# Kernel tuning notes

Measured on AMD Instinct MI355X. Metric: run time of the kernel, lower is better.

## Reference

```python
import jax, jax.numpy as jnp
import numpy as np

# conv hyperparams matching init_kwargs (kernel=3, stride=1, pad=1, dilation=1, dg=1)
KH = KW = 3
SH = SW = 1
PH = PW = 1
DH = DW = 1


def setup_inputs() -> dict:
    key = jax.random.key(0)
    k1, k2, k3 = jax.random.split(key, 3)
    N, C, H, W = 4, 64, 128, 128
    OC, KN = 64, KH * KW
    x = jax.random.normal(k1, (N, C, H, W), jnp.float32)
    # offset channels: deformable_groups * kernel_n * 2, ordered (y, x) per point
    offset = jax.random.normal(k2, (N, KN * 2, H, W), jnp.float32)
    weight = jax.random.normal(k3, (OC, C, KN), jnp.float32) * 0.05
    return {"x": x, "offset": offset, "weight": weight}


def _bilinear(img, ix, iy):
    # img: (C, H, W); ix, iy: (KN, OH, OW) pixel coords; align_corners=True, zeros padding
    H, W = img.shape[1], img.shape[2]
    x0 = jnp.floor(ix)
    y0 = jnp.floor(iy)
    x1 = x0 + 1.0
    y1 = y0 + 1.0
    wx1 = ix - x0
    wx0 = 1.0 - wx1
    wy1 = iy - y0
    wy0 = 1.0 - wy1

    def gather(xc, yc, w):
        xi = jnp.clip(xc, 0, W - 1).astype(jnp.int32)
        yi = jnp.clip(yc, 0, H - 1).astype(jnp.int32)
        m = ((xc >= 0) & (xc <= W - 1) & (yc >= 0) & (yc <= H - 1)).astype(img.dtype)
        return img[:, yi, xi] * (w * m)[None]  # (C, KN, OH, OW)

    return (gather(x0, y0, wx0 * wy0) + gather(x1, y0, wx1 * wy0)
            + gather(x0, y1, wx0 * wy1) + gather(x1, y1, wx1 * wy1))


def reference(x, offset, weight):
    N, C, H, W = x.shape
    KN = weight.shape[2]
    OH, OW = offset.shape[2], offset.shape[3]
    half_h = (H - 1) / 2.0
    half_w = (W - 1) / 2.0
    # base mesh in normalized [-1,1] coords (same for every kernel point, per source)
    ys = jnp.arange(OH, dtype=x.dtype) * SH - PH + ((KH - 1) // 2) * DH
    xs = jnp.arange(OW, dtype=x.dtype) * SW - PW + ((KW - 1) // 2) * DW
    base_gy = (ys - half_h) / half_h  # (OH,)
    base_gx = (xs - half_w) / half_w  # (OW,)
    off = offset.reshape(N, KN, 2, OH, OW)
    gy = base_gy[None, None, :, None] + off[:, :, 0] / half_h  # (N, KN, OH, OW)
    gx = base_gx[None, None, None, :] + off[:, :, 1] / half_w
    # back to pixel coords (align_corners=True)
    ix = (gx + 1.0) * half_w
    iy = (gy + 1.0) * half_h
    sampled = jax.vmap(_bilinear)(x, ix, iy)  # (N, C, KN, OH, OW)
    # weight (OC, C, KN) contracted over (C, KN); note: source forward never adds bias
    out = jnp.einsum('oik,nikhw->nohw', weight, sampled)
    return out
```

## Files before the change

kernel.cpp:

```cpp
#include <hip/hip_runtime.h>
#include <hip/hip_bf16.h>


#define NB 4
#define CI 64
#define HH 128
#define WW 128
#define OCH 64
#define KNN 9
#define HW (HH * WW)

typedef unsigned int u32;
typedef unsigned short u16;
typedef __attribute__((ext_vector_type(8))) short bf16x8;
typedef __attribute__((ext_vector_type(4))) float f32x4;

typedef const __attribute__((address_space(1))) u32* gas_ptr;
typedef __attribute__((address_space(3))) u32* las_ptr;

__device__ inline u16 f2bf(float f) {
    u32 u = __float_as_uint(f);
    return (u16)((u + 0x7fffu + ((u >> 16) & 1u)) >> 16);
}
__device__ inline u32 pk2(float lo, float hi) {
    return (u32)f2bf(lo) | ((u32)f2bf(hi) << 16);
}
__device__ inline void up2(u32 u, float& lo, float& hi) {
    lo = __uint_as_float(u << 16);
    hi = __uint_as_float(u & 0xffff0000u);
}
__device__ inline void gload_lds16(const u16* g, u16* s) {
    __builtin_amdgcn_global_load_lds((gas_ptr)g, (las_ptr)s, 16, 0, 0);
}

__global__ __launch_bounds__(256) void prep_kernel(const float* __restrict__ x,
                                                   const float* __restrict__ w,
                                                   u16* __restrict__ xT,
                                                   u16* __restrict__ wf) {
    __shared__ float T[64 * 68];
    const int tid = threadIdx.x;
    if (blockIdx.x < NB * 256) {
        const int n = blockIdx.x >> 8;
        const int hw0 = (blockIdx.x & 255) << 6;
#pragma unroll
        for (int jj = 0; jj < 4; jj++) {
            int c = (tid >> 4) + (jj << 4);
            int hwq = (tid & 15) << 2;
            float4 v = *(const float4*)&x[(((n << 6) + c) << 14) + hw0 + hwq];
            *(float4*)&T[c * 68 + hwq] = v;
        }
        __syncthreads();
        const int hw_l = tid >> 2;
        const int cb = (tid & 3) << 4;
        u32 ou[8];
#pragma unroll
        for (int k = 0; k < 8; k++) {
            ou[k] = pk2(T[(cb + 2 * k) * 68 + hw_l], T[(cb + 2 * k + 1) * 68 + hw_l]);
        }
        u16* dst = xT + ((size_t)((n << 14) + hw0 + hw_l) << 6) + cb;
        *(uint4*)dst = make_uint4(ou[0], ou[1], ou[2], ou[3]);
        *(uint4*)(dst + 8) = make_uint4(ou[4], ou[5], ou[6], ou[7]);
    } else {
        int i = (blockIdx.x - NB * 256) * 256 + tid;
        if (i < KNN * 2 * 4 * 64 * 8) {
            int j = i & 7, l = (i >> 3) & 63, strip = (i >> 9) & 3,
                chunk = (i >> 11) & 1, kn = i >> 12;
            int oc = strip * 16 + (l & 15);
            int c = chunk * 32 + ((l >> 4) & 3) * 8 + j;
            wf[i] = f2bf(w[(oc * CI + c) * KNN + kn]);
        }
    }
}

__global__ __launch_bounds__(256, 2) void dcn_main_kernel(const u16* __restrict__ xT,
                                                          const float* __restrict__ off,
                                                          const u16* __restrict__ wf,
                                                          float* __restrict__ out) {
    __shared__ __align__(16) u16 Abuf[KNN * 4096];
    const int tid = threadIdx.x;
    const int l = tid & 63;
    const int wv = tid >> 6;

    {
        const u16* g = wf + tid * 8;
        u16* s = Abuf + tid * 8;
#pragma unroll
        for (int i = 0; i < 18; i++) {
            gload_lds16(g + i * 2048, s + i * 2048);
        }
    }

    const int n = blockIdx.x >> 8;
    const int patch = blockIdx.x & 255;
    const int py = ((patch >> 4) << 3), px = ((patch & 15) << 3);
    const int qy = ((wv >> 1) << 2), qx = ((wv & 1) << 2);
    const int col = l & 15;
    const int oh = py + qy + (col >> 2);
    const int ow = px + qx + (col & 3);
    const int rr = (oh << 7) + ow;
    const int cbase = (l >> 4) << 3;
    const u16* xTn = xT + ((size_t)n << 20);
    const float* offn = off + n * (2 * KNN * HW);

    float offy[KNN], offx[KNN];
#pragma unroll
    for (int kn = 0; kn < KNN; kn++) {
        offy[kn] = offn[(2 * kn) * HW + rr];
        offx[kn] = offn[(2 * kn + 1) * HW + rr];
    }

    __syncthreads();

    f32x4 acc[4] = {{0, 0, 0, 0}, {0, 0, 0, 0}, {0, 0, 0, 0}, {0, 0, 0, 0}};

#pragma unroll
    for (int kn = 0; kn < KNN; kn++) {
        float iy = (float)oh + offy[kn], ix = (float)ow + offx[kn];
        float y0f = floorf(iy), x0f = floorf(ix);
        float wy1 = iy - y0f, wy0 = 1.f - wy1;
        float wx1 = ix - x0f, wx0 = 1.f - wx1;
        float my0 = (y0f >= 0.f && y0f <= 127.f) ? 1.f : 0.f;
        float my1 = (y0f >= -1.f && y0f <= 126.f) ? 1.f : 0.f;
        float mx0 = (x0f >= 0.f && x0f <= 127.f) ? 1.f : 0.f;
        float mx1 = (x0f >= -1.f && x0f <= 126.f) ? 1.f : 0.f;
        float W0 = wy0 * wx0 * my0 * mx0, W1 = wy0 * wx1 * my0 * mx1;
        float W2 = wy1 * wx0 * my1 * mx0, W3 = wy1 * wx1 * my1 * mx1;
        int y0 = min(max((int)y0f, 0), 127), y1 = min(max((int)y0f + 1, 0), 127);
        int x0 = min(max((int)x0f, 0), 127), x1 = min(max((int)x0f + 1, 0), 127);
        int O0 = ((y0 << 7) + x0) << 6, O1 = ((y0 << 7) + x1) << 6;
        int O2 = ((y1 << 7) + x0) << 6, O3 = ((y1 << 7) + x1) << 6;

#pragma unroll
        for (int ch = 0; ch < 2; ch++) {
            const int c = (ch << 5) + cbase;
            uint4 q0 = *(const uint4*)(xTn + O0 + c);
            uint4 q1 = *(const uint4*)(xTn + O1 + c);
            uint4 q2 = *(const uint4*)(xTn + O2 + c);
            uint4 q3 = *(const uint4*)(xTn + O3 + c);
            const u32* a0 = (const u32*)&q0;
            const u32* a1 = (const u32*)&q1;
            const u32* a2 = (const u32*)&q2;
            const u32* a3 = (const u32*)&q3;
            union { u32 u[4]; bf16x8 v; } B;
#pragma unroll
            for (int k = 0; k < 4; k++) {
                float p0l, p0h, p1l, p1h, p2l, p2h, p3l, p3h;
                up2(a0[k], p0l, p0h);
                up2(a1[k], p1l, p1h);
                up2(a2[k], p2l, p2h);
                up2(a3[k], p3l, p3h);
                float slo = p0l * W0 + p1l * W1 + p2l * W2 + p3l * W3;
                float shi = p0h * W0 + p1h * W1 + p2h * W2 + p3h * W3;
                B.u[k] = pk2(slo, shi);
            }
#pragma unroll
            for (int s = 0; s < 4; s++) {
                bf16x8 A = *(const bf16x8*)&Abuf[(((kn << 1) + ch) << 2 | s) * 512 + l * 8];
                acc[s] = __builtin_amdgcn_mfma_f32_16x16x32_bf16(A, B.v, acc[s], 0, 0, 0);
            }
        }
    }

    const int rq = l >> 4;
    float* op = out + ((size_t)(n * OCH) << 14);
#pragma unroll
    for (int s = 0; s < 4; s++) {
        const int ocb = (s << 4) + (rq << 2);
#pragma unroll
        for (int g = 0; g < 4; g++) {
            op[((ocb + g) << 14) + rr] = acc[s][g];
        }
    }
}

__global__ __launch_bounds__(256) void dcn_fallback_kernel(
    const float* __restrict__ x, const float* __restrict__ off,
    const float* __restrict__ w, float* __restrict__ out) {
    int p = blockIdx.x * blockDim.x + threadIdx.x;
    int n = p / HW, r = p % HW, oh = r / WW, ow = r % WW;
    float acc[OCH];
#pragma unroll
    for (int i = 0; i < OCH; i++) acc[i] = 0.f;
    const float* xn = x + n * (CI * HW);
    const float* offn = off + n * (2 * KNN * HW);
    for (int kn = 0; kn < KNN; kn++) {
        float iy = (float)oh + offn[(2 * kn) * HW + r];
        float ix = (float)ow + offn[(2 * kn + 1) * HW + r];
        float y0f = floorf(iy), x0f = floorf(ix);
        float wy1 = iy - y0f, wy0 = 1.f - wy1, wx1 = ix - x0f, wx0 = 1.f - wx1;
        float my0 = (y0f >= 0.f && y0f <= 127.f) ? 1.f : 0.f;
        float my1 = (y0f >= -1.f && y0f <= 126.f) ? 1.f : 0.f;
        float mx0 = (x0f >= 0.f && x0f <= 127.f) ? 1.f : 0.f;
        float mx1 = (x0f >= -1.f && x0f <= 126.f) ? 1.f : 0.f;
        float w00 = wy0 * wx0 * my0 * mx0, w01 = wy0 * wx1 * my0 * mx1;
        float w10 = wy1 * wx0 * my1 * mx0, w11 = wy1 * wx1 * my1 * mx1;
        int y0 = min(max((int)y0f, 0), 127), y1 = min(max((int)y0f + 1, 0), 127);
        int x0 = min(max((int)x0f, 0), 127), x1 = min(max((int)x0f + 1, 0), 127);
        int o00 = y0 * WW + x0, o01 = y0 * WW + x1, o10 = y1 * WW + x0, o11 = y1 * WW + x1;
        for (int c = 0; c < CI; c++) {
            const float* xc = xn + c * HW;
            float s = xc[o00] * w00 + xc[o01] * w01 + xc[o10] * w10 + xc[o11] * w11;
#pragma unroll
            for (int oc = 0; oc < OCH; oc++) acc[oc] += w[(oc * CI + c) * KNN + kn] * s;
        }
    }
    float* outp = out + n * (OCH * HW) + r;
#pragma unroll
    for (int oc = 0; oc < OCH; oc++) outp[oc * HW] = acc[oc];
}

extern "C" void kernel_launch(void* const* d_in, const int* in_sizes, int n_in,
                              void* d_out, int out_size, void* d_ws, size_t ws_size,
                              hipStream_t stream) {
    const float* x = (const float*)d_in[0];
    const float* off = (const float*)d_in[1];
    const float* w = (const float*)d_in[2];
    float* out = (float*)d_out;

    const size_t xT_elems = (size_t)NB * HW * CI;
    const size_t wf_elems = (size_t)KNN * 2 * 4 * 64 * 8;
    const size_t need = (xT_elems + wf_elems) * sizeof(u16);

    if (ws_size >= need) {
        u16* xT = (u16*)d_ws;
        u16* wfr = xT + xT_elems;
        const int wf_blocks = (int)((wf_elems + 255) / 256);
        prep_kernel<<<NB * 256 + wf_blocks, 256, 0, stream>>>(x, w, xT, wfr);
        dcn_main_kernel<<<NB * 256, 256, 0, stream>>>(xT, off, wfr, out);
    } else {
        dcn_fallback_kernel<<<(NB * HW) / 256, 256, 0, stream>>>(x, off, w, out);
    }
}
```

Baseline: 114.5 us.

## Drop LDS weight staging, read weights from global, raise occupancy, remap blocks to XCDs

```diff
diff --git a/kernel.cpp b/kernel.cpp
--- a/kernel.cpp
+++ b/kernel.cpp
@@ -15,9 +15,6 @@
 typedef __attribute__((ext_vector_type(8))) short bf16x8;
 typedef __attribute__((ext_vector_type(4))) float f32x4;
 
-typedef const __attribute__((address_space(1))) u32* gas_ptr;
-typedef __attribute__((address_space(3))) u32* las_ptr;
-
 __device__ inline u16 f2bf(float f) {
     u32 u = __float_as_uint(f);
     return (u16)((u + 0x7fffu + ((u >> 16) & 1u)) >> 16);
@@ -28,9 +25,6 @@
 __device__ inline void up2(u32 u, float& lo, float& hi) {
     lo = __uint_as_float(u << 16);
     hi = __uint_as_float(u & 0xffff0000u);
-}
-__device__ inline void gload_lds16(const u16* g, u16* s) {
-    __builtin_amdgcn_global_load_lds((gas_ptr)g, (las_ptr)s, 16, 0, 0);
 }
 
 __global__ __launch_bounds__(256) void prep_kernel(const float* __restrict__ x,
@@ -72,26 +66,18 @@
     }
 }
 
-__global__ __launch_bounds__(256, 2) void dcn_main_kernel(const u16* __restrict__ xT,
+__global__ __launch_bounds__(256, 4) void dcn_main_kernel(const u16* __restrict__ xT,
                                                           const float* __restrict__ off,
                                                           const u16* __restrict__ wf,
                                                           float* __restrict__ out) {
-    __shared__ __align__(16) u16 Abuf[KNN * 4096];
     const int tid = threadIdx.x;
     const int l = tid & 63;
     const int wv = tid >> 6;
 
-    {
-        const u16* g = wf + tid * 8;
-        u16* s = Abuf + tid * 8;
-#pragma unroll
-        for (int i = 0; i < 18; i++) {
-            gload_lds16(g + i * 2048, s + i * 2048);
-        }
-    }
-
-    const int n = blockIdx.x >> 8;
-    const int patch = blockIdx.x & 255;
+    const int b = blockIdx.x;
+    const int xcd = b & 7;
+    const int n = xcd >> 1;
+    const int patch = (b >> 3) + ((xcd & 1) << 7);
     const int py = ((patch >> 4) << 3), px = ((patch & 15) << 3);
     const int qy = ((wv >> 1) << 2), qx = ((wv & 1) << 2);
     const int col = l & 15;
@@ -101,21 +87,20 @@
     const int cbase = (l >> 4) << 3;
     const u16* xTn = xT + ((size_t)n << 20);
     const float* offn = off + n * (2 * KNN * HW);
-
-    float offy[KNN], offx[KNN];
-#pragma unroll
+    const bf16x8* wfv = (const bf16x8*)wf;
+
+    f32x4 acc[4] = {{0, 0, 0, 0}, {0, 0, 0, 0}, {0, 0, 0, 0}, {0, 0, 0, 0}};
+
+    float oy = offn[0 * HW + rr];
+    float ox = offn[1 * HW + rr];
+
+#pragma unroll 1
     for (int kn = 0; kn < KNN; kn++) {
-        offy[kn] = offn[(2 * kn) * HW + rr];
-        offx[kn] = offn[(2 * kn + 1) * HW + rr];
-    }
-
-    __syncthreads();
-
-    f32x4 acc[4] = {{0, 0, 0, 0}, {0, 0, 0, 0}, {0, 0, 0, 0}, {0, 0, 0, 0}};
-
-#pragma unroll
-    for (int kn = 0; kn < KNN; kn++) {
-        float iy = (float)oh + offy[kn], ix = (float)ow + offx[kn];
+        const int knx = (kn + 1 < KNN) ? kn + 1 : kn;
+        float noy = offn[(2 * knx) * HW + rr];
+        float nox = offn[(2 * knx + 1) * HW + rr];
+
+        float iy = (float)oh + oy, ix = (float)ow + ox;
         float y0f = floorf(iy), x0f = floorf(ix);
         float wy1 = iy - y0f, wy0 = 1.f - wy1;
         float wx1 = ix - x0f, wx0 = 1.f - wx1;
@@ -127,20 +112,28 @@
         float W2 = wy1 * wx0 * my1 * mx0, W3 = wy1 * wx1 * my1 * mx1;
         int y0 = min(max((int)y0f, 0), 127), y1 = min(max((int)y0f + 1, 0), 127);
         int x0 = min(max((int)x0f, 0), 127), x1 = min(max((int)x0f + 1, 0), 127);
-        int O0 = ((y0 << 7) + x0) << 6, O1 = ((y0 << 7) + x1) << 6;
-        int O2 = ((y1 << 7) + x0) << 6, O3 = ((y1 << 7) + x1) << 6;
-
+        const u16* p0 = xTn + (((y0 << 7) + x0) << 6) + cbase;
+        const u16* p1 = xTn + (((y0 << 7) + x1) << 6) + cbase;
+        const u16* p2 = xTn + (((y1 << 7) + x0) << 6) + cbase;
+        const u16* p3 = xTn + (((y1 << 7) + x1) << 6) + cbase;
+
+        uint4 q[8];
+        q[0] = *(const uint4*)(p0);
+        q[1] = *(const uint4*)(p1);
+        q[2] = *(const uint4*)(p2);
+        q[3] = *(const uint4*)(p3);
+        q[4] = *(const uint4*)(p0 + 32);
+        q[5] = *(const uint4*)(p1 + 32);
+        q[6] = *(const uint4*)(p2 + 32);
+        q[7] = *(const uint4*)(p3 + 32);
+
+        const int base = kn << 3;
 #pragma unroll
         for (int ch = 0; ch < 2; ch++) {
-            const int c = (ch << 5) + cbase;
-            uint4 q0 = *(const uint4*)(xTn + O0 + c);
-            uint4 q1 = *(const uint4*)(xTn + O1 + c);
-            uint4 q2 = *(const uint4*)(xTn + O2 + c);
-            uint4 q3 = *(const uint4*)(xTn + O3 + c);
-            const u32* a0 = (const u32*)&q0;
-            const u32* a1 = (const u32*)&q1;
-            const u32* a2 = (const u32*)&q2;
-            const u32* a3 = (const u32*)&q3;
+            const u32* a0 = (const u32*)&q[ch * 4 + 0];
+            const u32* a1 = (const u32*)&q[ch * 4 + 1];
+            const u32* a2 = (const u32*)&q[ch * 4 + 2];
+            const u32* a3 = (const u32*)&q[ch * 4 + 3];
             union { u32 u[4]; bf16x8 v; } B;
 #pragma unroll
             for (int k = 0; k < 4; k++) {
@@ -155,10 +148,12 @@
             }
 #pragma unroll
             for (int s = 0; s < 4; s++) {
-                bf16x8 A = *(const bf16x8*)&Abuf[(((kn << 1) + ch) << 2 | s) * 512 + l * 8];
+                bf16x8 A = wfv[((base + (ch << 2) + s) << 6) + l];
                 acc[s] = __builtin_amdgcn_mfma_f32_16x16x32_bf16(A, B.v, acc[s], 0, 0, 0);
             }
         }
+        oy = noy;
+        ox = nox;
     }
 
     const int rq = l >> 4;
```

Result: slower. 120.5 us (+5.2%).

## Software-pipeline bilinear gathers two kernel points ahead and remap blocks to XCDs

Applied to the files above, without the earlier changes.

```diff
diff --git a/kernel.cpp b/kernel.cpp
--- a/kernel.cpp
+++ b/kernel.cpp
@@ -90,8 +90,10 @@
         }
     }
 
-    const int n = blockIdx.x >> 8;
-    const int patch = blockIdx.x & 255;
+    const int b = blockIdx.x;
+    const int xcd = b & 7;
+    const int n = xcd >> 1;
+    const int patch = (b >> 3) + ((xcd & 1) << 7);
     const int py = ((patch >> 4) << 3), px = ((patch & 15) << 3);
     const int qy = ((wv >> 1) << 2), qx = ((wv & 1) << 2);
     const int col = l & 15;
@@ -113,8 +115,11 @@
 
     f32x4 acc[4] = {{0, 0, 0, 0}, {0, 0, 0, 0}, {0, 0, 0, 0}, {0, 0, 0, 0}};
 
-#pragma unroll
-    for (int kn = 0; kn < KNN; kn++) {
+    float W[2][4];
+    uint4 Q[2][8];
+
+    auto coords_and_issue = [&](int kn) {
+        const int p = kn & 1;
         float iy = (float)oh + offy[kn], ix = (float)ow + offx[kn];
         float y0f = floorf(iy), x0f = floorf(ix);
         float wy1 = iy - y0f, wy0 = 1.f - wy1;
@@ -123,41 +128,65 @@
         float my1 = (y0f >= -1.f && y0f <= 126.f) ? 1.f : 0.f;
         float mx0 = (x0f >= 0.f && x0f <= 127.f) ? 1.f : 0.f;
         float mx1 = (x0f >= -1.f && x0f <= 126.f) ? 1.f : 0.f;
-        float W0 = wy0 * wx0 * my0 * mx0, W1 = wy0 * wx1 * my0 * mx1;
-        float W2 = wy1 * wx0 * my1 * mx0, W3 = wy1 * wx1 * my1 * mx1;
+        W[p][0] = wy0 * wx0 * my0 * mx0;
+        W[p][1] = wy0 * wx1 * my0 * mx1;
+        W[p][2] = wy1 * wx0 * my1 * mx0;
+        W[p][3] = wy1 * wx1 * my1 * mx1;
         int y0 = min(max((int)y0f, 0), 127), y1 = min(max((int)y0f + 1, 0), 127);
         int x0 = min(max((int)x0f, 0), 127), x1 = min(max((int)x0f + 1, 0), 127);
-        int O0 = ((y0 << 7) + x0) << 6, O1 = ((y0 << 7) + x1) << 6;
-        int O2 = ((y1 << 7) + x0) << 6, O3 = ((y1 << 7) + x1) << 6;
-
-#pragma unroll
-        for (int ch = 0; ch < 2; ch++) {
-            const int c = (ch << 5) + cbase;
-            uint4 q0 = *(const uint4*)(xTn + O0 + c);
-            uint4 q1 = *(const uint4*)(xTn + O1 + c);
-            uint4 q2 = *(const uint4*)(xTn + O2 + c);
-            uint4 q3 = *(const uint4*)(xTn + O3 + c);
-            const u32* a0 = (const u32*)&q0;
-            const u32* a1 = (const u32*)&q1;
-            const u32* a2 = (const u32*)&q2;
-            const u32* a3 = (const u32*)&q3;
-            union { u32 u[4]; bf16x8 v; } B;
-#pragma unroll
-            for (int k = 0; k < 4; k++) {
-                float p0l, p0h, p1l, p1h, p2l, p2h, p3l, p3h;
-                up2(a0[k], p0l, p0h);
-                up2(a1[k], p1l, p1h);
-                up2(a2[k], p2l, p2h);
-                up2(a3[k], p3l, p3h);
-                float slo = p0l * W0 + p1l * W1 + p2l * W2 + p3l * W3;
-                float shi = p0h * W0 + p1h * W1 + p2h * W2 + p3h * W3;
-                B.u[k] = pk2(slo, shi);
-            }
-#pragma unroll
-            for (int s = 0; s < 4; s++) {
-                bf16x8 A = *(const bf16x8*)&Abuf[(((kn << 1) + ch) << 2 | s) * 512 + l * 8];
-                acc[s] = __builtin_amdgcn_mfma_f32_16x16x32_bf16(A, B.v, acc[s], 0, 0, 0);
-            }
+        const u16* p0 = xTn + (((y0 << 7) + x0) << 6) + cbase;
+        const u16* p1 = xTn + (((y0 << 7) + x1) << 6) + cbase;
+        const u16* p2 = xTn + (((y1 << 7) + x0) << 6) + cbase;
+        const u16* p3 = xTn + (((y1 << 7) + x1) << 6) + cbase;
+        Q[p][0] = *(const uint4*)(p0);
+        Q[p][1] = *(const uint4*)(p1);
+        Q[p][2] = *(const uint4*)(p2);
+        Q[p][3] = *(const uint4*)(p3);
+        Q[p][4] = *(const uint4*)(p0 + 32);
+        Q[p][5] = *(const uint4*)(p1 + 32);
+        Q[p][6] = *(const uint4*)(p2 + 32);
+        Q[p][7] = *(const uint4*)(p3 + 32);
+    };
+
+    coords_and_issue(0);
+    coords_and_issue(1);
+
+#pragma unroll 1
+    for (int kn = 0; kn < KNN; kn++) {
+        const int p = kn & 1;
+        union { u32 u[4]; bf16x8 v; } B0, B1;
+#pragma unroll
+        for (int k = 0; k < 4; k++) {
+            float a0l, a0h, a1l, a1h, a2l, a2h, a3l, a3h;
+            up2(((const u32*)&Q[p][0])[k], a0l, a0h);
+            up2(((const u32*)&Q[p][1])[k], a1l, a1h);
+            up2(((const u32*)&Q[p][2])[k], a2l, a2h);
+            up2(((const u32*)&Q[p][3])[k], a3l, a3h);
+            float slo = a0l * W[p][0] + a1l * W[p][1] + a2l * W[p][2] + a3l * W[p][3];
+            float shi = a0h * W[p][0] + a1h * W[p][1] + a2h * W[p][2] + a3h * W[p][3];
+            B0.u[k] = pk2(slo, shi);
+        }
+#pragma unroll
+        for (int k = 0; k < 4; k++) {
+            float a0l, a0h, a1l, a1h, a2l, a2h, a3l, a3h;
+            up2(((const u32*)&Q[p][4])[k], a0l, a0h);
+            up2(((const u32*)&Q[p][5])[k], a1l, a1h);
+            up2(((const u32*)&Q[p][6])[k], a2l, a2h);
+            up2(((const u32*)&Q[p][7])[k], a3l, a3h);
+            float slo = a0l * W[p][0] + a1l * W[p][1] + a2l * W[p][2] + a3l * W[p][3];
+            float shi = a0h * W[p][0] + a1h * W[p][1] + a2h * W[p][2] + a3h * W[p][3];
+            B1.u[k] = pk2(slo, shi);
+        }
+        if (kn + 2 < KNN) coords_and_issue(kn + 2);
+#pragma unroll
+        for (int s = 0; s < 4; s++) {
+            bf16x8 A0 = *(const bf16x8*)&Abuf[(((kn << 1) + 0) << 2 | s) * 512 + l * 8];
+            acc[s] = __builtin_amdgcn_mfma_f32_16x16x32_bf16(A0, B0.v, acc[s], 0, 0, 0);
+        }
+#pragma unroll
+        for (int s = 0; s < 4; s++) {
+            bf16x8 A1 = *(const bf16x8*)&Abuf[(((kn << 1) + 1) << 2 | s) * 512 + l * 8];
+            acc[s] = __builtin_amdgcn_mfma_f32_16x16x32_bf16(A1, B1.v, acc[s], 0, 0, 0);
         }
     }
 
```

Measured after the change: 175.8 us. 1.54x slower.

## Stage a 16x16 input halo tile in LDS and read weights from global

Applied to the files above, without the earlier changes.

```diff
diff --git a/kernel.cpp b/kernel.cpp
--- a/kernel.cpp
+++ b/kernel.cpp
@@ -15,9 +15,6 @@
 typedef __attribute__((ext_vector_type(8))) short bf16x8;
 typedef __attribute__((ext_vector_type(4))) float f32x4;
 
-typedef const __attribute__((address_space(1))) u32* gas_ptr;
-typedef __attribute__((address_space(3))) u32* las_ptr;
-
 __device__ inline u16 f2bf(float f) {
     u32 u = __float_as_uint(f);
     return (u16)((u + 0x7fffu + ((u >> 16) & 1u)) >> 16);
@@ -28,9 +25,6 @@
 __device__ inline void up2(u32 u, float& lo, float& hi) {
     lo = __uint_as_float(u << 16);
     hi = __uint_as_float(u & 0xffff0000u);
-}
-__device__ inline void gload_lds16(const u16* g, u16* s) {
-    __builtin_amdgcn_global_load_lds((gas_ptr)g, (las_ptr)s, 16, 0, 0);
 }
 
 __global__ __launch_bounds__(256) void prep_kernel(const float* __restrict__ x,
@@ -72,35 +66,42 @@
     }
 }
 
-__global__ __launch_bounds__(256, 2) void dcn_main_kernel(const u16* __restrict__ xT,
+__global__ __launch_bounds__(256, 3) void dcn_main_kernel(const u16* __restrict__ xT,
                                                           const float* __restrict__ off,
                                                           const u16* __restrict__ wf,
                                                           float* __restrict__ out) {
-    __shared__ __align__(16) u16 Abuf[KNN * 4096];
+    __shared__ __align__(16) u16 tile[256 * 72];
     const int tid = threadIdx.x;
     const int l = tid & 63;
     const int wv = tid >> 6;
 
+    const int b = blockIdx.x;
+    const int xcd = b & 7;
+    const int n = xcd >> 1;
+    const int patch = (b >> 3) + ((xcd & 1) << 7);
+    const int py = ((patch >> 4) << 3), px = ((patch & 15) << 3);
+    const int ty = min(max(py - 4, 0), HH - 16);
+    const int tx = min(max(px - 4, 0), WW - 16);
+
+    const u16* xTn = xT + ((size_t)n << 20);
+    const float* offn = off + n * (2 * KNN * HW);
+
     {
-        const u16* g = wf + tid * 8;
-        u16* s = Abuf + tid * 8;
-#pragma unroll
-        for (int i = 0; i < 18; i++) {
-            gload_lds16(g + i * 2048, s + i * 2048);
-        }
-    }
-
-    const int n = blockIdx.x >> 8;
-    const int patch = blockIdx.x & 255;
-    const int py = ((patch >> 4) << 3), px = ((patch & 15) << 3);
+        const int tr = tid >> 4, tc = tid & 15;
+        const u16* src = xTn + ((((ty + tr) << 7) + (tx + tc)) << 6);
+        u16* dst = &tile[tid * 72];
+#pragma unroll
+        for (int j = 0; j < 8; j++) {
+            *(uint4*)(dst + j * 8) = *(const uint4*)(src + j * 8);
+        }
+    }
+
     const int qy = ((wv >> 1) << 2), qx = ((wv & 1) << 2);
     const int col = l & 15;
     const int oh = py + qy + (col >> 2);
     const int ow = px + qx + (col & 3);
     const int rr = (oh << 7) + ow;
     const int cbase = (l >> 4) << 3;
-    const u16* xTn = xT + ((size_t)n << 20);
-    const float* offn = off + n * (2 * KNN * HW);
 
     float offy[KNN], offx[KNN];
 #pragma unroll
@@ -111,6 +112,7 @@
 
     __syncthreads();
 
+    const bf16x8* wfv = (const bf16x8*)wf;
     f32x4 acc[4] = {{0, 0, 0, 0}, {0, 0, 0, 0}, {0, 0, 0, 0}, {0, 0, 0, 0}};
 
 #pragma unroll
@@ -127,20 +129,41 @@
         float W2 = wy1 * wx0 * my1 * mx0, W3 = wy1 * wx1 * my1 * mx1;
         int y0 = min(max((int)y0f, 0), 127), y1 = min(max((int)y0f + 1, 0), 127);
         int x0 = min(max((int)x0f, 0), 127), x1 = min(max((int)x0f + 1, 0), 127);
-        int O0 = ((y0 << 7) + x0) << 6, O1 = ((y0 << 7) + x1) << 6;
-        int O2 = ((y1 << 7) + x0) << 6, O3 = ((y1 << 7) + x1) << 6;
+
+        const int dy0 = min(max(y0 - ty, 0), 15), dy1 = min(max(y1 - ty, 0), 15);
+        const int dx0 = min(max(x0 - tx, 0), 15), dx1 = min(max(x1 - tx, 0), 15);
+        const int p00 = (dy0 << 4) + dx0, p01 = (dy0 << 4) + dx1;
+        const int p10 = (dy1 << 4) + dx0, p11 = (dy1 << 4) + dx1;
+        const bool oot = (y0 < ty) | (y1 > ty + 15) | (x0 < tx) | (x1 > tx + 15);
+
+        uint4 q[8];
+        q[0] = *(const uint4*)&tile[p00 * 72 + cbase];
+        q[1] = *(const uint4*)&tile[p01 * 72 + cbase];
+        q[2] = *(const uint4*)&tile[p10 * 72 + cbase];
+        q[3] = *(const uint4*)&tile[p11 * 72 + cbase];
+        q[4] = *(const uint4*)&tile[p00 * 72 + cbase + 32];
+        q[5] = *(const uint4*)&tile[p01 * 72 + cbase + 32];
+        q[6] = *(const uint4*)&tile[p10 * 72 + cbase + 32];
+        q[7] = *(const uint4*)&tile[p11 * 72 + cbase + 32];
+        if (oot) {
+            const int O0 = ((y0 << 7) + x0) << 6, O1 = ((y0 << 7) + x1) << 6;
+            const int O2 = ((y1 << 7) + x0) << 6, O3 = ((y1 << 7) + x1) << 6;
+            q[0] = *(const uint4*)(xTn + O0 + cbase);
+            q[1] = *(const uint4*)(xTn + O1 + cbase);
+            q[2] = *(const uint4*)(xTn + O2 + cbase);
+            q[3] = *(const uint4*)(xTn + O3 + cbase);
+            q[4] = *(const uint4*)(xTn + O0 + cbase + 32);
+            q[5] = *(const uint4*)(xTn + O1 + cbase + 32);
+            q[6] = *(const uint4*)(xTn + O2 + cbase + 32);
+            q[7] = *(const uint4*)(xTn + O3 + cbase + 32);
+        }
 
 #pragma unroll
         for (int ch = 0; ch < 2; ch++) {
-            const int c = (ch << 5) + cbase;
-            uint4 q0 = *(const uint4*)(xTn + O0 + c);
-            uint4 q1 = *(const uint4*)(xTn + O1 + c);
-            uint4 q2 = *(const uint4*)(xTn + O2 + c);
-            uint4 q3 = *(const uint4*)(xTn + O3 + c);
-            const u32* a0 = (const u32*)&q0;
-            const u32* a1 = (const u32*)&q1;
-            const u32* a2 = (const u32*)&q2;
-            const u32* a3 = (const u32*)&q3;
+            const u32* a0 = (const u32*)&q[ch * 4 + 0];
+            const u32* a1 = (const u32*)&q[ch * 4 + 1];
+            const u32* a2 = (const u32*)&q[ch * 4 + 2];
+            const u32* a3 = (const u32*)&q[ch * 4 + 3];
             union { u32 u[4]; bf16x8 v; } B;
 #pragma unroll
             for (int k = 0; k < 4; k++) {
@@ -155,7 +178,7 @@
             }
 #pragma unroll
             for (int s = 0; s < 4; s++) {
-                bf16x8 A = *(const bf16x8*)&Abuf[(((kn << 1) + ch) << 2 | s) * 512 + l * 8];
+                bf16x8 A = wfv[((((kn << 1) + ch) << 2) + s) * 64 + l];
                 acc[s] = __builtin_amdgcn_mfma_f32_16x16x32_bf16(A, B.v, acc[s], 0, 0, 0);
             }
         }
```

Result: faster. 102.3 us (-10.7%).
